# Performance work log

Hardware: AMD Instinct MI355X
Metric: run time of the kernel (lower is better)

Reference implementation:

```python
import jax, jax.numpy as jnp
import numpy as np

# Graph geometry: G complete graphs (molecules) of n nodes each.
N_PER_G, G, DEG = 64, 256, 16
H, D = 8, 8
IN_DIM = H * D      # 64
EDGE_DIM = 64
N = N_PER_G * G                      # 16384 nodes
EF = G * N_PER_G * N_PER_G           # 1,048,576 full edges
ES = G * N_PER_G * DEG               # 262,144 sparse edges
SCALE = float(np.sqrt(D))


def _edges():
    n = N_PER_G
    # full graph: all (i -> j) pairs per block, edge id = b*n*n + i*n + j
    ij = np.arange(n * n)
    i, j = ij // n, ij % n
    b = np.arange(G)[:, None]
    src_full = (b * n + i[None, :]).reshape(-1).astype(np.int32)
    dst_full = (b * n + j[None, :]).reshape(-1).astype(np.int32)
    # sparse graph: each dst j receives from DEG distinct sources (j+1..j+DEG mod n)
    jj = np.arange(n)[:, None]
    kk = np.arange(DEG)[None, :]
    ii = (jj + 1 + kk) % n
    eid_block = (ii * n + jj).reshape(-1)                 # [n*DEG]
    sparse_eid = (np.arange(G)[:, None] * n * n + eid_block[None, :]).reshape(-1).astype(np.int32)
    return jnp.asarray(src_full), jnp.asarray(dst_full), jnp.asarray(sparse_eid)


def setup_inputs() -> dict:
    key = jax.random.key(0)
    ks = jax.random.split(key, 16)
    w = lambda k, shape, s=0.05: s * jax.random.normal(k, shape, jnp.float32)
    src_full, dst_full, sparse_eid = _edges()
    return dict(
        h=jax.random.normal(ks[0], (N, IN_DIM), jnp.float32),
        e=jax.random.normal(ks[1], (ES, EDGE_DIM), jnp.float32),
        adj2=jax.random.uniform(ks[2], (EF,), jnp.float32),
        rel_pos_3d=jax.random.normal(ks[3], (EF, H), jnp.float32),
        Wq=w(ks[4], (H * D, IN_DIM)), bq=jnp.zeros((H * D,), jnp.float32),
        Wk=w(ks[5], (H * D, IN_DIM)), bk=jnp.zeros((H * D,), jnp.float32),
        Wv=w(ks[6], (H * D, IN_DIM)), bv=jnp.zeros((H * D,), jnp.float32),
        Wpe=w(ks[7], (H, EDGE_DIM)), bpe=jnp.zeros((H,), jnp.float32),
        Wap=w(ks[8], (EDGE_DIM, H)), bap=jnp.zeros((EDGE_DIM,), jnp.float32),
        Wo=w(ks[9], (H * D, H * D)), bo=jnp.zeros((H * D,), jnp.float32),
        Woe=w(ks[10], (EDGE_DIM, EDGE_DIM)), boe=jnp.zeros((EDGE_DIM,), jnp.float32),
        src_full=src_full, dst_full=dst_full, sparse_eid=sparse_eid,
    )


def reference(h, e, adj2, rel_pos_3d, Wq, bq, Wk, bk, Wv, bv, Wpe, bpe,
              Wap, bap, Wo, bo, Woe, boe, src_full, dst_full, sparse_eid):
    Qh = (h @ Wq.T + bq).reshape(N, H, D)
    Kh = (h @ Wk.T + bk).reshape(N, H, D)
    Vh = (h @ Wv.T + bv).reshape(N, H, D)
    proj_e = e @ Wpe.T + bpe                                   # [ES, H]
    # edge-wise QK dot (src=K, dst=Q), scaled, then gaussian-decay + rel-pos bias
    score = jnp.sum(Kh[src_full] * Qh[dst_full], axis=-1) / SCALE   # [EF, H]
    score = score * adj2[:, None] + rel_pos_3d                      # [EF, H]
    # gather sparse-subgraph scores, project for edge output, add proj_e bias
    sc_sp = score[sparse_eid]                                        # [ES, H]
    e_out_raw = sc_sp @ Wap.T + bap                                  # [ES, EDGE_DIM]
    score = score.at[sparse_eid].set(sc_sp + proj_e)
    # edge softmax over incoming edges of each destination node
    logits = jnp.clip(score, -5.0, 5.0)
    m = jax.ops.segment_max(logits, dst_full, num_segments=N)
    ex = jnp.exp(logits - m[dst_full])
    den = jax.ops.segment_sum(ex, dst_full, num_segments=N)
    attn = ex / den[dst_full]                                        # [EF, H]
    # weighted scatter-sum of source values
    wV = jax.ops.segment_sum(Vh[src_full] * attn[..., None], dst_full, num_segments=N)
    h_out = wV.reshape(N, H * D) @ Wo.T + bo
    e_out = (e_out_raw + e) @ Woe.T + boe
    return h_out, e_out
```

## Files before the change

kernel.cpp:

```cpp
#include <hip/hip_runtime.h>


__global__ __launch_bounds__(512, 2) void qkvpe_kernel(
    const float* __restrict__ h,
    const float* __restrict__ e,
    const float* __restrict__ Wq, const float* __restrict__ bq,
    const float* __restrict__ Wk, const float* __restrict__ bk,
    const float* __restrict__ Wv, const float* __restrict__ bv,
    const float* __restrict__ Wpe, const float* __restrict__ bpe,
    float* __restrict__ Qs, float* __restrict__ Ks, float* __restrict__ Vs,
    float* __restrict__ PEs)
{
    const int t = threadIdx.x;
    if (blockIdx.x < 256) {
        const int b    = blockIdx.x;
        const int lane = t & 63;
        const int wu   = __builtin_amdgcn_readfirstlane(t >> 6);
        const float* hrow = h + (size_t)(b * 64 + lane) * 64;
        float accQ[8], accK[8], accV[8];
        #pragma unroll
        for (int cc = 0; cc < 8; ++cc) {
            const int c = wu * 8 + cc;
            accQ[cc] = bq[c]; accK[cc] = bk[c]; accV[cc] = bv[c];
        }
        #pragma unroll 1
        for (int k0 = 0; k0 < 4; ++k0) {
            float hv[16];
            #pragma unroll
            for (int u = 0; u < 4; ++u) {
                const float4 x = ((const float4*)hrow)[k0 * 4 + u];
                hv[u*4+0] = x.x; hv[u*4+1] = x.y; hv[u*4+2] = x.z; hv[u*4+3] = x.w;
            }
            #pragma unroll
            for (int cc = 0; cc < 8; ++cc) {
                const int c = wu * 8 + cc;
                const float* wq  = Wq + c * 64 + k0 * 16;
                const float* wk  = Wk + c * 64 + k0 * 16;
                const float* wvp = Wv + c * 64 + k0 * 16;
                #pragma unroll
                for (int k = 0; k < 16; ++k) {
                    accQ[cc] = fmaf(hv[k], wq[k],  accQ[cc]);
                    accK[cc] = fmaf(hv[k], wk[k],  accK[cc]);
                    accV[cc] = fmaf(hv[k], wvp[k], accV[cc]);
                }
            }
        }
        const size_t o = (size_t)(b * 64 + lane) * 64 + wu * 8;
        *(float4*)(Qs + o)     = make_float4(accQ[0], accQ[1], accQ[2], accQ[3]);
        *(float4*)(Qs + o + 4) = make_float4(accQ[4], accQ[5], accQ[6], accQ[7]);
        *(float4*)(Ks + o)     = make_float4(accK[0], accK[1], accK[2], accK[3]);
        *(float4*)(Ks + o + 4) = make_float4(accK[4], accK[5], accK[6], accK[7]);
        *(float4*)(Vs + o)     = make_float4(accV[0], accV[1], accV[2], accV[3]);
        *(float4*)(Vs + o + 4) = make_float4(accV[4], accV[5], accV[6], accV[7]);
    } else {
        const int row = (blockIdx.x - 256) * 512 + t;
        const float* erow = e + (size_t)row * 64;
        float acc[8];
        #pragma unroll
        for (int h2 = 0; h2 < 8; ++h2) acc[h2] = bpe[h2];
        #pragma unroll 1
        for (int k0 = 0; k0 < 4; ++k0) {
            float ev[16];
            #pragma unroll
            for (int u = 0; u < 4; ++u) {
                const float4 x = ((const float4*)erow)[k0 * 4 + u];
                ev[u*4+0] = x.x; ev[u*4+1] = x.y; ev[u*4+2] = x.z; ev[u*4+3] = x.w;
            }
            #pragma unroll
            for (int h2 = 0; h2 < 8; ++h2) {
                const float* wp = Wpe + h2 * 64 + k0 * 16;
                #pragma unroll
                for (int k = 0; k < 16; ++k)
                    acc[h2] = fmaf(ev[k], wp[k], acc[h2]);
            }
        }
        float* p0 = PEs + (size_t)row * 8;
        *(float4*)(p0)     = make_float4(acc[0], acc[1], acc[2], acc[3]);
        *(float4*)(p0 + 4) = make_float4(acc[4], acc[5], acc[6], acc[7]);
    }
}

__global__ __launch_bounds__(1024, 2) void attn_kernel(
    const float* __restrict__ Qs, const float* __restrict__ Ks,
    const float* __restrict__ Vs, const float* __restrict__ PEs,
    const float* __restrict__ adj2,
    const float* __restrict__ rel,
    const float* __restrict__ Wo, const float* __restrict__ bo,
    float* __restrict__ h_out,
    float* __restrict__ scsp)
{
    __shared__ float shK[64 * 64];
    __shared__ float shV[64 * 64];
    __shared__ float shPE[512 * 8];

    const int b2   = blockIdx.x;
    const int b    = b2 >> 1;
    const int joff = (b2 & 1) << 5;
    const int t    = threadIdx.x;

    const int j_local = t >> 5;
    const int hh      = (t >> 2) & 7;
    const int q4      = t & 3;
    const int j       = joff + j_local;

    {
        const int r  = t >> 4;
        const int gh = t & 15;
        const int g  = gh >> 1, lo = (gh & 1) * 4;
        const int d  = r * 64 + ((g ^ (r & 7)) << 3) + lo;
        const int so = r * 64 + g * 8 + lo;
        shK[d + 0] = Ks[(size_t)b * 4096 + so + 0];
        shK[d + 1] = Ks[(size_t)b * 4096 + so + 1];
        shK[d + 2] = Ks[(size_t)b * 4096 + so + 2];
        shK[d + 3] = Ks[(size_t)b * 4096 + so + 3];
        shV[d + 0] = Vs[(size_t)b * 4096 + so + 0];
        shV[d + 1] = Vs[(size_t)b * 4096 + so + 1];
        shV[d + 2] = Vs[(size_t)b * 4096 + so + 2];
        shV[d + 3] = Vs[(size_t)b * 4096 + so + 3];
        *(float4*)&shPE[t * 4] =
            *(const float4*)(PEs + ((size_t)b * 1024 + joff * 16) * 8 + t * 4);
    }
    float q[8];
    {
        const float* qp = Qs + (size_t)(b * 64 + j) * 64 + hh * 8;
        const float4 a = *(const float4*)qp;
        const float4 c = *(const float4*)(qp + 4);
        q[0]=a.x; q[1]=a.y; q[2]=a.z; q[3]=a.w;
        q[4]=c.x; q[5]=c.y; q[6]=c.z; q[7]=c.w;
    }
    __syncthreads();

    float den = 0.f;
    float wv[8] = {0.f,0.f,0.f,0.f,0.f,0.f,0.f,0.f};
    const float* adjB = adj2 + (size_t)b * 4096 + j;
    const float* relB = rel  + ((size_t)b * 4096 + j) * 8 + hh;
    const float inv_scale = 0.35355339059327379f;
    #pragma unroll 4
    for (int it = 0; it < 16; ++it) {
        const int i  = (q4 << 4) + it;
        const float a2 = adjB[(size_t)i * 64];
        const float rp = relB[(size_t)i * 512];
        const int kb = i * 64 + ((hh ^ (i & 7)) << 3);
        const float4 kA = *(const float4*)&shK[kb];
        const float4 kB = *(const float4*)&shK[kb + 4];
        float s;
        s = kA.x * q[0];
        s = fmaf(kA.y, q[1], s); s = fmaf(kA.z, q[2], s); s = fmaf(kA.w, q[3], s);
        s = fmaf(kB.x, q[4], s); s = fmaf(kB.y, q[5], s); s = fmaf(kB.z, q[6], s);
        s = fmaf(kB.w, q[7], s);
        s = fmaf(s * inv_scale, a2, rp);
        const int kidx = (i - j - 1) & 63;
        if (kidx < 16) {
            const int x = (j_local * 16 + kidx) * 8 + hh;
            const float pe = shPE[x];
            shPE[x] = s;
            s += pe;
        }
        s = fminf(fmaxf(s, -5.f), 5.f);
        const float ex = __expf(s);
        den += ex;
        const float4 vA = *(const float4*)&shV[kb];
        const float4 vB = *(const float4*)&shV[kb + 4];
        wv[0] = fmaf(ex, vA.x, wv[0]); wv[1] = fmaf(ex, vA.y, wv[1]);
        wv[2] = fmaf(ex, vA.z, wv[2]); wv[3] = fmaf(ex, vA.w, wv[3]);
        wv[4] = fmaf(ex, vB.x, wv[4]); wv[5] = fmaf(ex, vB.y, wv[5]);
        wv[6] = fmaf(ex, vB.z, wv[6]); wv[7] = fmaf(ex, vB.w, wv[7]);
    }
    den += __shfl_xor(den, 1);
    den += __shfl_xor(den, 2);
    #pragma unroll
    for (int u = 0; u < 8; ++u) {
        wv[u] += __shfl_xor(wv[u], 1);
        wv[u] += __shfl_xor(wv[u], 2);
    }
    __syncthreads();

    {
        const int row = t >> 1, pp = t & 1;
        *(float4*)(scsp + (size_t)((size_t)b * 1024 + joff * 16 + row) * 8 + pp * 4) =
            *(const float4*)&shPE[row * 8 + pp * 4];
    }
    if (q4 == 0) {
        const float id = 1.f / den;
        float* wp = &shK[j_local * 64 + hh * 8];
        *(float4*)(wp)     = make_float4(wv[0]*id, wv[1]*id, wv[2]*id, wv[3]*id);
        *(float4*)(wp + 4) = make_float4(wv[4]*id, wv[5]*id, wv[6]*id, wv[7]*id);
    }
    __syncthreads();

    {
        const int rl = t >> 5;
        const int c0 = (t & 31) * 2;
        float acc[2];
        acc[0] = bo[c0]; acc[1] = bo[c0 + 1];
        #pragma unroll 1
        for (int k0 = 0; k0 < 4; ++k0) {
            float tv[16];
            #pragma unroll
            for (int u = 0; u < 4; ++u) {
                const float4 x = *(const float4*)&shK[rl * 64 + k0 * 16 + u * 4];
                tv[u*4+0] = x.x; tv[u*4+1] = x.y; tv[u*4+2] = x.z; tv[u*4+3] = x.w;
            }
            #pragma unroll
            for (int u = 0; u < 2; ++u) {
                const float* wo = Wo + (c0 + u) * 64 + k0 * 16;
                #pragma unroll
                for (int k = 0; k < 16; ++k)
                    acc[u] = fmaf(tv[k], wo[k], acc[u]);
            }
        }
        float* orow = h_out + (size_t)(b * 64 + joff + rl) * 64 + c0;
        *(float2*)orow = make_float2(acc[0], acc[1]);
    }
}

__global__ void prep_kernel(const float* __restrict__ Wap, const float* __restrict__ bap,
                            const float* __restrict__ Woe, const float* __restrict__ boe,
                            float* __restrict__ M2)
{
    const int t = blockIdx.x * 64 + threadIdx.x;
    if (t < 512) {
        const int c = t >> 3, hq = t & 7;
        float s = 0.f;
        #pragma unroll 8
        for (int k = 0; k < 64; ++k) s = fmaf(Woe[c * 64 + k], Wap[k * 8 + hq], s);
        M2[t] = s;
    } else if (t < 576) {
        const int c = t - 512;
        float s = boe[c];
        #pragma unroll 8
        for (int k = 0; k < 64; ++k) s = fmaf(bap[k], Woe[c * 64 + k], s);
        M2[512 + c] = s;
    }
}

__global__ __launch_bounds__(256, 2) void eout_kernel(
    const float* __restrict__ e,
    const float* __restrict__ scsp,
    const float* __restrict__ Woe,
    const float* __restrict__ M2g,
    float* __restrict__ e_out)
{
    __shared__ float shE[64 * 64];
    __shared__ float shS[64 * 8];

    const int t    = threadIdx.x;
    const int base = blockIdx.x * 64;

    {
        const int r = t >> 2, qq = t & 3;
        const float* ep = e + (size_t)(base + r) * 64 + qq * 16;
        #pragma unroll
        for (int u = 0; u < 4; ++u) {
            const float4 x = ((const float4*)ep)[u];
            const int cc = qq * 4 + u;
            *(float4*)&shE[r * 64 + ((cc ^ (r & 15)) << 2)] = x;
        }
    }
    if (t < 128) {
        const int r = t >> 1, pp = t & 1;
        *(float4*)&shS[r * 8 + pp * 4] =
            *(const float4*)(scsp + (size_t)(base + r) * 8 + pp * 4);
    }
    __syncthreads();

    const int w = __builtin_amdgcn_readfirstlane(t >> 6);
    const int r = t & 63;

    float ev[64];
    #pragma unroll
    for (int v = 0; v < 16; ++v) {
        const float4 x = *(const float4*)&shE[r * 64 + ((v ^ (r & 15)) << 2)];
        ev[v*4+0] = x.x; ev[v*4+1] = x.y; ev[v*4+2] = x.z; ev[v*4+3] = x.w;
    }
    float sc[8];
    {
        const float4 a  = *(const float4*)&shS[r * 8];
        const float4 c4 = *(const float4*)&shS[r * 8 + 4];
        sc[0]=a.x; sc[1]=a.y; sc[2]=a.z; sc[3]=a.w;
        sc[4]=c4.x; sc[5]=c4.y; sc[6]=c4.z; sc[7]=c4.w;
    }
    float acc[16];
    #pragma unroll
    for (int u = 0; u < 16; ++u) {
        const int c = w * 16 + u;
        float s = M2g[512 + c];
        #pragma unroll
        for (int hq = 0; hq < 8; ++hq)
            s = fmaf(sc[hq], M2g[c * 8 + hq], s);
        acc[u] = s;
    }
    #pragma unroll
    for (int u = 0; u < 16; ++u) {
        const float* wr = Woe + (w * 16 + u) * 64;
        #pragma unroll
        for (int k = 0; k < 64; ++k)
            acc[u] = fmaf(ev[k], wr[k], acc[u]);
    }
    float* orow = e_out + (size_t)(base + r) * 64 + w * 16;
    #pragma unroll
    for (int u = 0; u < 4; ++u)
        *(float4*)&orow[u * 4] =
            make_float4(acc[u*4+0], acc[u*4+1], acc[u*4+2], acc[u*4+3]);
}

extern "C" void kernel_launch(void* const* d_in, const int* in_sizes, int n_in,
                              void* d_out, int out_size, void* d_ws, size_t ws_size,
                              hipStream_t stream) {
    const float* h    = (const float*)d_in[0];
    const float* e    = (const float*)d_in[1];
    const float* adj2 = (const float*)d_in[2];
    const float* rel  = (const float*)d_in[3];
    const float* Wq   = (const float*)d_in[4];  const float* bq  = (const float*)d_in[5];
    const float* Wk   = (const float*)d_in[6];  const float* bk  = (const float*)d_in[7];
    const float* Wv   = (const float*)d_in[8];  const float* bv  = (const float*)d_in[9];
    const float* Wpe  = (const float*)d_in[10]; const float* bpe = (const float*)d_in[11];
    const float* Wap  = (const float*)d_in[12]; const float* bap = (const float*)d_in[13];
    const float* Wo   = (const float*)d_in[14]; const float* bo  = (const float*)d_in[15];
    const float* Woe  = (const float*)d_in[16]; const float* boe = (const float*)d_in[17];

    float* out  = (float*)d_out;
    float* hout = out;
    float* eout = out + 16384 * 64;
    float* Qs   = eout;
    float* Ks   = eout + 1048576;
    float* Vs   = eout + 2097152;
    float* PEs  = eout + 3145728;
    float* ws   = (float*)d_ws;
    float* scsp = ws;
    float* M2g  = ws + 2097152;

    prep_kernel<<<dim3(9), dim3(64), 0, stream>>>(Wap, bap, Woe, boe, M2g);
    qkvpe_kernel<<<dim3(768), dim3(512), 0, stream>>>(
        h, e, Wq, bq, Wk, bk, Wv, bv, Wpe, bpe, Qs, Ks, Vs, PEs);
    attn_kernel<<<dim3(512), dim3(1024), 0, stream>>>(
        Qs, Ks, Vs, PEs, adj2, rel, Wo, bo, hout, scsp);
    eout_kernel<<<dim3(4096), dim3(256), 0, stream>>>(e, scsp, Woe, M2g, eout);
}
```

Measured before the change: 145.3 us.

## Stage rel/adj tiles in shared memory and add transposed-weight e_out kernel

The attention kernel now loads rel_pos and adj2 for each 16-row chunk cooperatively into shared memory with coalesced float4 loads, replacing strided per-thread global loads. This adds extra barriers per chunk. A new eoutT kernel uses a prep-built transposed weight matrix (Woe plus the folded Wap and bias rows) so weight reads are contiguous per k, and it reads e from a padded transposed shared tile. The old eout kernel is kept as a fallback when the workspace is too small, with its register usage reduced by chunking ev.

New measurement: 139.3 us. 1.04x faster.

```diff
diff --git a/kernel.cpp b/kernel.cpp
--- a/kernel.cpp
+++ b/kernel.cpp
@@ -80,6 +80,15 @@
     }
 }
 
+#define STAGE_RELADJ(c4_) {                                                   \
+    const int il_ = t >> 6;                                                   \
+    *(float4*)&shRel[il_ * 264 + (t & 63) * 4] =                              \
+        *(const float4*)(relBase + ((c4_) * 16 + il_) * 512 + (t & 63) * 4);  \
+    if (t < 512) {                                                            \
+        const int ia_ = t >> 5, jl_ = t & 31;                                 \
+        shAdj[ia_ * 36 + jl_] = adjBase[((c4_) * 16 + ia_) * 64 + jl_];       \
+    } }
+
 __global__ __launch_bounds__(1024, 2) void attn_kernel(
     const float* __restrict__ Qs, const float* __restrict__ Ks,
     const float* __restrict__ Vs, const float* __restrict__ PEs,
@@ -92,6 +101,8 @@
     __shared__ float shK[64 * 64];
     __shared__ float shV[64 * 64];
     __shared__ float shPE[512 * 8];
+    __shared__ float shRel[16 * 264];
+    __shared__ float shAdj[16 * 36];
 
     const int b2   = blockIdx.x;
     const int b    = b2 >> 1;
@@ -102,6 +113,9 @@
     const int hh      = (t >> 2) & 7;
     const int q4      = t & 3;
     const int j       = joff + j_local;
+
+    const float* relBase = rel  + (size_t)b * 32768 + joff * 8;
+    const float* adjBase = adj2 + (size_t)b * 4096  + joff;
 
     {
         const int r  = t >> 4;
@@ -120,6 +134,7 @@
         *(float4*)&shPE[t * 4] =
             *(const float4*)(PEs + ((size_t)b * 1024 + joff * 16) * 8 + t * 4);
     }
+    STAGE_RELADJ(0);
     float q[8];
     {
         const float* qp = Qs + (size_t)(b * 64 + j) * 64 + hh * 8;
@@ -128,43 +143,49 @@
         q[0]=a.x; q[1]=a.y; q[2]=a.z; q[3]=a.w;
         q[4]=c.x; q[5]=c.y; q[6]=c.z; q[7]=c.w;
     }
-    __syncthreads();
 
     float den = 0.f;
     float wv[8] = {0.f,0.f,0.f,0.f,0.f,0.f,0.f,0.f};
-    const float* adjB = adj2 + (size_t)b * 4096 + j;
-    const float* relB = rel  + ((size_t)b * 4096 + j) * 8 + hh;
     const float inv_scale = 0.35355339059327379f;
-    #pragma unroll 4
-    for (int it = 0; it < 16; ++it) {
-        const int i  = (q4 << 4) + it;
-        const float a2 = adjB[(size_t)i * 64];
-        const float rp = relB[(size_t)i * 512];
-        const int kb = i * 64 + ((hh ^ (i & 7)) << 3);
-        const float4 kA = *(const float4*)&shK[kb];
-        const float4 kB = *(const float4*)&shK[kb + 4];
-        float s;
-        s = kA.x * q[0];
-        s = fmaf(kA.y, q[1], s); s = fmaf(kA.z, q[2], s); s = fmaf(kA.w, q[3], s);
-        s = fmaf(kB.x, q[4], s); s = fmaf(kB.y, q[5], s); s = fmaf(kB.z, q[6], s);
-        s = fmaf(kB.w, q[7], s);
-        s = fmaf(s * inv_scale, a2, rp);
-        const int kidx = (i - j - 1) & 63;
-        if (kidx < 16) {
-            const int x = (j_local * 16 + kidx) * 8 + hh;
-            const float pe = shPE[x];
-            shPE[x] = s;
-            s += pe;
-        }
-        s = fminf(fmaxf(s, -5.f), 5.f);
-        const float ex = __expf(s);
-        den += ex;
-        const float4 vA = *(const float4*)&shV[kb];
-        const float4 vB = *(const float4*)&shV[kb + 4];
-        wv[0] = fmaf(ex, vA.x, wv[0]); wv[1] = fmaf(ex, vA.y, wv[1]);
-        wv[2] = fmaf(ex, vA.z, wv[2]); wv[3] = fmaf(ex, vA.w, wv[3]);
-        wv[4] = fmaf(ex, vB.x, wv[4]); wv[5] = fmaf(ex, vB.y, wv[5]);
-        wv[6] = fmaf(ex, vB.z, wv[6]); wv[7] = fmaf(ex, vB.w, wv[7]);
+    #pragma unroll 1
+    for (int c4 = 0; c4 < 4; ++c4) {
+        __syncthreads();
+        #pragma unroll
+        for (int it2 = 0; it2 < 4; ++it2) {
+            const int il = it2 * 4 + q4;
+            const int i  = c4 * 16 + il;
+            const float a2 = shAdj[il * 36 + j_local];
+            const float rp = shRel[il * 264 + j_local * 8 + hh];
+            const int kb = i * 64 + ((hh ^ (i & 7)) << 3);
+            const float4 kA = *(const float4*)&shK[kb];
+            const float4 kB = *(const float4*)&shK[kb + 4];
+            float s;
+            s = kA.x * q[0];
+            s = fmaf(kA.y, q[1], s); s = fmaf(kA.z, q[2], s); s = fmaf(kA.w, q[3], s);
+            s = fmaf(kB.x, q[4], s); s = fmaf(kB.y, q[5], s); s = fmaf(kB.z, q[6], s);
+            s = fmaf(kB.w, q[7], s);
+            s = fmaf(s * inv_scale, a2, rp);
+            const int kidx = (i - j - 1) & 63;
+            if (kidx < 16) {
+                const int x = (j_local * 16 + kidx) * 8 + hh;
+                const float pe = shPE[x];
+                shPE[x] = s;
+                s += pe;
+            }
+            s = fminf(fmaxf(s, -5.f), 5.f);
+            const float ex = __expf(s);
+            den += ex;
+            const float4 vA = *(const float4*)&shV[kb];
+            const float4 vB = *(const float4*)&shV[kb + 4];
+            wv[0] = fmaf(ex, vA.x, wv[0]); wv[1] = fmaf(ex, vA.y, wv[1]);
+            wv[2] = fmaf(ex, vA.z, wv[2]); wv[3] = fmaf(ex, vA.w, wv[3]);
+            wv[4] = fmaf(ex, vB.x, wv[4]); wv[5] = fmaf(ex, vB.y, wv[5]);
+            wv[6] = fmaf(ex, vB.z, wv[6]); wv[7] = fmaf(ex, vB.w, wv[7]);
+        }
+        if (c4 < 3) {
+            __syncthreads();
+            STAGE_RELADJ(c4 + 1);
+        }
     }
     den += __shfl_xor(den, 1);
     den += __shfl_xor(den, 2);
@@ -216,22 +237,111 @@
 
 __global__ void prep_kernel(const float* __restrict__ Wap, const float* __restrict__ bap,
                             const float* __restrict__ Woe, const float* __restrict__ boe,
-                            float* __restrict__ M2)
+                            float* __restrict__ M2, float* __restrict__ Tm, int hasT)
 {
-    const int t = blockIdx.x * 64 + threadIdx.x;
-    if (t < 512) {
-        const int c = t >> 3, hq = t & 7;
+    const int tg = blockIdx.x * 64 + threadIdx.x;
+    if (tg < 512) {
+        const int c = tg >> 3, hq = tg & 7;
         float s = 0.f;
         #pragma unroll 8
         for (int k = 0; k < 64; ++k) s = fmaf(Woe[c * 64 + k], Wap[k * 8 + hq], s);
-        M2[t] = s;
-    } else if (t < 576) {
-        const int c = t - 512;
+        M2[tg] = s;
+    } else if (tg < 576) {
+        const int c = tg - 512;
         float s = boe[c];
         #pragma unroll 8
         for (int k = 0; k < 64; ++k) s = fmaf(bap[k], Woe[c * 64 + k], s);
         M2[512 + c] = s;
-    }
+    } else if (hasT && tg < 576 + 73 * 64) {
+        const int idx = tg - 576;
+        const int k = idx >> 6, c = idx & 63;
+        float v;
+        if (k < 64) {
+            v = Woe[c * 64 + k];
+        } else if (k < 72) {
+            const int hq = k - 64;
+            v = 0.f;
+            #pragma unroll 8
+            for (int kk = 0; kk < 64; ++kk)
+                v = fmaf(Woe[c * 64 + kk], Wap[kk * 8 + hq], v);
+        } else {
+            v = boe[c];
+            #pragma unroll 8
+            for (int kk = 0; kk < 64; ++kk)
+                v = fmaf(bap[kk], Woe[c * 64 + kk], v);
+        }
+        Tm[k * 64 + c] = v;
+    }
+}
+
+__global__ __launch_bounds__(256, 2) void eoutT_kernel(
+    const float* __restrict__ e,
+    const float* __restrict__ scsp,
+    const float* __restrict__ Tm,
+    float* __restrict__ e_out)
+{
+    __shared__ float shET[64 * 67];
+    __shared__ float shS[64 * 8];
+
+    const int t    = threadIdx.x;
+    const int base = blockIdx.x * 64;
+
+    {
+        const int r0 = t >> 2, qq = t & 3;
+        const float* ep = e + (size_t)(base + r0) * 64 + qq * 16;
+        #pragma unroll
+        for (int v = 0; v < 4; ++v) {
+            const float4 x = ((const float4*)ep)[v];
+            const int c = qq * 16 + v * 4;
+            shET[(c + 0) * 67 + r0] = x.x;
+            shET[(c + 1) * 67 + r0] = x.y;
+            shET[(c + 2) * 67 + r0] = x.z;
+            shET[(c + 3) * 67 + r0] = x.w;
+        }
+    }
+    if (t < 128) {
+        const int r = t >> 1, pp = t & 1;
+        *(float4*)&shS[r * 8 + pp * 4] =
+            *(const float4*)(scsp + (size_t)(base + r) * 8 + pp * 4);
+    }
+    __syncthreads();
+
+    const int w = __builtin_amdgcn_readfirstlane(t >> 6);
+    const int r = t & 63;
+
+    float sc[8];
+    {
+        const float4 a  = *(const float4*)&shS[r * 8];
+        const float4 c4 = *(const float4*)&shS[r * 8 + 4];
+        sc[0]=a.x; sc[1]=a.y; sc[2]=a.z; sc[3]=a.w;
+        sc[4]=c4.x; sc[5]=c4.y; sc[6]=c4.z; sc[7]=c4.w;
+    }
+    float acc[16];
+    {
+        const float* bcw = Tm + 72 * 64 + w * 16;
+        #pragma unroll
+        for (int u = 0; u < 16; ++u) acc[u] = bcw[u];
+    }
+    #pragma unroll
+    for (int k = 0; k < 64; ++k) {
+        const float evk = shET[k * 67 + r];
+        const float* wk = Tm + k * 64 + w * 16;
+        #pragma unroll
+        for (int u = 0; u < 16; ++u)
+            acc[u] = fmaf(evk, wk[u], acc[u]);
+    }
+    #pragma unroll
+    for (int hq = 0; hq < 8; ++hq) {
+        const float* wk = Tm + (64 + hq) * 64 + w * 16;
+        #pragma unroll
+        for (int u = 0; u < 16; ++u)
+            acc[u] = fmaf(sc[hq], wk[u], acc[u]);
+    }
+    float* orow = e_out + (size_t)(base + r) * 64 + w * 16;
+    #pragma unroll
+    for (int u = 0; u < 4; ++u)
+        *(float4*)&orow[u * 4] =
+            make_float4(acc[u*4+0], acc[u*4+1], acc[u*4+2], acc[u*4+3]);
 }
 
 __global__ __launch_bounds__(256, 2) void eout_kernel(
@@ -243,10 +353,8 @@
 {
     __shared__ float shE[64 * 64];
     __shared__ float shS[64 * 8];
-
     const int t    = threadIdx.x;
     const int base = blockIdx.x * 64;
-
     {
         const int r = t >> 2, qq = t & 3;
         const float* ep = e + (size_t)(base + r) * 64 + qq * 16;
@@ -263,16 +371,8 @@
             *(const float4*)(scsp + (size_t)(base + r) * 8 + pp * 4);
     }
     __syncthreads();
-
     const int w = __builtin_amdgcn_readfirstlane(t >> 6);
     const int r = t & 63;
-
-    float ev[64];
-    #pragma unroll
-    for (int v = 0; v < 16; ++v) {
-        const float4 x = *(const float4*)&shE[r * 64 + ((v ^ (r & 15)) << 2)];
-        ev[v*4+0] = x.x; ev[v*4+1] = x.y; ev[v*4+2] = x.z; ev[v*4+3] = x.w;
-    }
     float sc[8];
     {
         const float4 a  = *(const float4*)&shS[r * 8];
@@ -291,11 +391,21 @@
         acc[u] = s;
     }
     #pragma unroll
-    for (int u = 0; u < 16; ++u) {
-        const float* wr = Woe + (w * 16 + u) * 64;
-        #pragma unroll
-        for (int k = 0; k < 64; ++k)
-            acc[u] = fmaf(ev[k], wr[k], acc[u]);
+    for (int k0 = 0; k0 < 4; ++k0) {
+        float ev[16];
+        #pragma unroll
+        for (int v = 0; v < 4; ++v) {
+            const int cc = k0 * 4 + v;
+            const float4 x = *(const float4*)&shE[r * 64 + ((cc ^ (r & 15)) << 2)];
+            ev[v*4+0] = x.x; ev[v*4+1] = x.y; ev[v*4+2] = x.z; ev[v*4+3] = x.w;
+        }
+        #pragma unroll
+        for (int u = 0; u < 16; ++u) {
+            const float* wr = Woe + (w * 16 + u) * 64 + k0 * 16;
+            #pragma unroll
+            for (int k = 0; k < 16; ++k)
+                acc[u] = fmaf(ev[k], wr[k], acc[u]);
+        }
     }
     float* orow = e_out + (size_t)(base + r) * 64 + w * 16;
     #pragma unroll
@@ -329,11 +439,16 @@
     float* ws   = (float*)d_ws;
     float* scsp = ws;
     float* M2g  = ws + 2097152;
-
-    prep_kernel<<<dim3(9), dim3(64), 0, stream>>>(Wap, bap, Woe, boe, M2g);
+    float* Tm   = ws + 2098176;
+    const int hasT = (ws_size >= (size_t)(2098176 + 73 * 64) * sizeof(float)) ? 1 : 0;
+
+    prep_kernel<<<dim3(82), dim3(64), 0, stream>>>(Wap, bap, Woe, boe, M2g, Tm, hasT);
     qkvpe_kernel<<<dim3(768), dim3(512), 0, stream>>>(
         h, e, Wq, bq, Wk, bk, Wv, bv, Wpe, bpe, Qs, Ks, Vs, PEs);
     attn_kernel<<<dim3(512), dim3(1024), 0, stream>>>(
         Qs, Ks, Vs, PEs, adj2, rel, Wo, bo, hout, scsp);
-    eout_kernel<<<dim3(4096), dim3(256), 0, stream>>>(e, scsp, Woe, M2g, eout);
-}
+    if (hasT)
+        eoutT_kernel<<<dim3(4096), dim3(256), 0, stream>>>(e, scsp, Tm, eout);
+    else
+        eout_kernel<<<dim3(4096), dim3(256), 0, stream>>>(e, scsp, Woe, M2g, eout);
+}
```
